# Kernel optimization log

Hardware: AMD Instinct MI355X
Metric: run time of the kernel (lower is better)

## Reference

```python
import jax, jax.numpy as jnp
import numpy as np

B, S, H, A = 64, 200, 256, 16
CAPS_LAYERS = 3
NEG = -1e9
LN_EPS = 1e-12


def _layernorm(x, g, b):
    mu = jnp.mean(x, axis=-1, keepdims=True)
    var = jnp.mean(jnp.square(x - mu), axis=-1, keepdims=True)
    return (x - mu) / jnp.sqrt(var + LN_EPS) * g + b


def setup_inputs() -> dict:
    key = jax.random.key(0)
    ks = jax.random.split(key, 10)
    s = 0.02  # initializer_range
    return {
        "item_emb": jax.random.normal(ks[0], (B, S, H), jnp.float32),
        "item_seq": jax.random.randint(ks[1], (B, S), 0, 50000),
        "time_seq": jax.random.randint(ks[2], (B, S, 2), 0, 14),
        "W_lin": s * jax.random.normal(ks[3], (H, H), jnp.float32),
        "b_lin": jnp.zeros((H,), jnp.float32),
        "aspect_embs": s * jax.random.normal(ks[4], (A, H), jnp.float32),
        "pos_emb": s * jax.random.normal(ks[5], (S, H), jnp.float32),
        "tdt_emb": s * jax.random.normal(ks[6], (14, H), jnp.float32),
        "tdn_emb": s * jax.random.normal(ks[7], (14, H), jnp.float32),
        "Wa1": s * jax.random.normal(ks[8], (H, H), jnp.float32),
        "ba1": jnp.zeros((H,), jnp.float32),
        "Wa2": s * jax.random.normal(ks[9], (H,), jnp.float32),
        "ba2": jnp.zeros((1,), jnp.float32),
        "ln_g": jnp.ones((H,), jnp.float32),
        "ln_b": jnp.zeros((H,), jnp.float32),
    }


def reference(item_emb, item_seq, time_seq, W_lin, b_lin, aspect_embs,
              pos_emb, tdt_emb, tdn_emb, Wa1, ba1, Wa2, ba2, ln_g, ln_b):
    b, s = item_emb.shape[0], item_emb.shape[1]
    pad = item_seq == 0  # [B,S]

    # ---- TimeAwareAttention (seq_output has a singleton neighbor dim in torch) ----
    td = tdt_emb[time_seq[:, :, 0]] + tdn_emb[time_seq[:, :, 1]]       # [B,S,H]
    tma_in = pos_emb[None, :s] + item_emb + td                          # [B,S,H]
    h = tma_in @ Wa1 + ba1
    h = jnp.where(h >= 0, h, 0.01 * h)                                  # LeakyReLU
    w = h @ Wa2 + ba2[0]                                                # [B,S]
    w = jnp.where(pad, NEG, w)
    tma = jax.nn.softmax(w, axis=-1)                                    # [B,S]

    # ---- gating (eval: clean gates) ----
    gates = jnp.einsum('bsh,ah->bsa', item_emb, aspect_embs)            # [B,S,A]
    idx = jnp.argmax(gates, axis=-1)                                    # topk k=1, [B,S]

    src = jnp.where(pad, 0.0, 1.0)
    counts = jnp.zeros((b, A), jnp.float32).at[jnp.arange(b)[:, None], idx].add(src)
    aspect_mask = counts == 0                                           # [B,A]

    # ---- item transform (dropout = identity in eval) ----
    moe = _layernorm(jnp.tanh(item_emb @ W_lin + b_lin) + item_emb, ln_g, ln_b)  # [B,S,H]

    # ---- capsule routing ----
    bij = gates
    cap = jnp.broadcast_to(aspect_embs[None], (b, A, H))
    for _ in range(CAPS_LAYERS):
        cij = jnp.where(aspect_mask[:, None, :], NEG, bij)
        cij = jax.nn.softmax(cij, axis=-1)
        cij = jnp.where(pad[:, :, None], 0.0, cij)                      # [B,S,A]
        cap = jnp.einsum('bsa,bsh,bs->bah', cij, moe, tma)              # [B,A,H]
        n2 = jnp.sum(jnp.square(cap), axis=-1, keepdims=True)
        cap = n2 / (1.0 + n2) / jnp.sqrt(n2 + 1e-9) * cap               # squash
        bij = bij + jnp.einsum('bsh,bah->bsa', moe, cap)

    # ---- gather activated interests / activation positions ----
    activated = cap[jnp.arange(b)[:, None], idx]                        # [B,S,H]
    seq_pos = jnp.where(pad, 0, jnp.arange(1, s + 1)[None, :]).astype(jnp.float32)
    act_mat = jnp.full((b, s, A), -1.0, jnp.float32)
    act_mat = act_mat.at[jnp.arange(b)[:, None], jnp.arange(s)[None, :], idx].set(seq_pos)
    act_mat = jnp.where(pad[:, :, None], -1.0, act_mat)
    max_pos = jnp.max(act_mat, axis=1)                                  # [B,A]
    aspects_item_idx = jnp.where(max_pos > -1.0, max_pos - 1.0, max_pos)

    gates_sm = jax.nn.softmax(gates, axis=-1)
    return (cap, gates_sm, aspect_mask, activated, aspects_item_idx, idx[:, :, None])
```

## Files before the change

### kernel.cpp

```cpp
#include <hip/hip_runtime.h>

#define B_ 64
#define S_ 200
#define H_ 256
#define A_ 16
#define M_ (B_*S_)
#define NEGV (-1000000000.0f)

typedef unsigned short ushortT;
typedef __attribute__((ext_vector_type(8))) short short8;
typedef __attribute__((ext_vector_type(4))) float f32x4;

__device__ __forceinline__ ushortT bf16u(float f) {
  unsigned int u = __builtin_bit_cast(unsigned int, f);
  unsigned int r = (u + 0x7fffu + ((u >> 16) & 1u)) >> 16;
  return (ushortT)r;
}
__device__ __forceinline__ float bf2f(ushortT u) {
  unsigned int v = ((unsigned int)u) << 16;
  return __builtin_bit_cast(float, v);
}

__global__ __launch_bounds__(256) void prep_kernel(
    const float* __restrict__ item, const float* __restrict__ Wa1,
    const float* __restrict__ W_lin, const float* __restrict__ asp,
    ushortT* __restrict__ Wa1T, ushortT* __restrict__ WlinT,
    float* __restrict__ graw, float* __restrict__ gates_sm,
    float* __restrict__ idxf)
{
  const int blk = blockIdx.x;
  const int t = threadIdx.x;

  if (blk >= 800) {
    __shared__ float T[64*65];
    int wsel = (blk - 800) >> 4;
    int tile = (blk - 800) & 15;
    const float* W = wsel ? W_lin : Wa1;
    ushortT* WT = wsel ? WlinT : Wa1T;
    int tr = (tile >> 2) * 64, tc = (tile & 3) * 64;
    #pragma unroll
    for (int p = 0; p < 16; ++p) {
      int r = p*4 + (t >> 6);
      int c = t & 63;
      T[c*65 + r] = W[(tr + r)*H_ + tc + c];
    }
    __syncthreads();
    #pragma unroll
    for (int p = 0; p < 16; ++p) {
      int n = p*4 + (t >> 6);
      int k = t & 63;
      WT[(tc + n)*H_ + tr + k] = bf16u(T[n*65 + k]);
    }
    return;
  }

  __shared__ float aspl[16*260];
  __shared__ float gL[16*20];

  const int m0 = blk * 16;
  #pragma unroll
  for (int i = 0; i < 4; ++i) {
    int e = t + 256*i;
    int r = e >> 6, c = e & 63;
    *(float4*)&aspl[r*260 + 4*c] = *(const float4*)&asp[r*H_ + 4*c];
  }
  __syncthreads();

  {
    int r = t >> 4, a = t & 15;
    int m = m0 + r;
    float g = 0.f;
    #pragma unroll 4
    for (int k4 = 0; k4 < 64; ++k4) {
      float4 xv = *(const float4*)&item[(size_t)m*H_ + 4*k4];
      float4 av = *(const float4*)&aspl[a*260 + 4*k4];
      g += xv.x*av.x + xv.y*av.y + xv.z*av.z + xv.w*av.w;
    }
    gL[r*20 + a] = g;
  }
  __syncthreads();
  if (t < 64) {
    int r = t >> 2, q = t & 3;
    float4 gv;
    gv.x = gL[r*20 + 4*q + 0]; gv.y = gL[r*20 + 4*q + 1];
    gv.z = gL[r*20 + 4*q + 2]; gv.w = gL[r*20 + 4*q + 3];
    *(float4*)&graw[(m0+r)*A_ + 4*q] = gv;
  }
  if (t < 16) {
    int r = t;
    float best = gL[r*20]; int bi = 0;
    float mx = gL[r*20];
    #pragma unroll
    for (int a = 1; a < 16; ++a) {
      float v = gL[r*20 + a];
      if (v > best) { best = v; bi = a; }
      mx = fmaxf(mx, v);
    }
    idxf[m0 + r] = (float)bi;
    float ex[16]; float sm = 0.f;
    #pragma unroll
    for (int a = 0; a < 16; ++a) { ex[a] = expf(gL[r*20 + a] - mx); sm += ex[a]; }
    float inv = 1.f / sm;
    #pragma unroll
    for (int a = 0; a < 16; ++a) gates_sm[(m0+r)*A_ + a] = ex[a]*inv;
  }
}

#define ASTR 280
#define BSTR 40
__global__ __launch_bounds__(512) void gemm_kernel(
    const float* __restrict__ item, const int* __restrict__ iseq,
    const int* __restrict__ tseq, const float* __restrict__ pos,
    const float* __restrict__ tdt, const float* __restrict__ tdn,
    const ushortT* __restrict__ Wa1T, const ushortT* __restrict__ WlinT,
    const float* __restrict__ ba1, const float* __restrict__ Wa2,
    const float* __restrict__ ba2, const float* __restrict__ b_lin,
    const float* __restrict__ g_ln, const float* __restrict__ b_ln,
    float* __restrict__ w_out, ushortT* __restrict__ moe_outB)
{
  __shared__ ushortT Atma[64*ASTR];
  __shared__ ushortT Aitm[64*ASTR];
  __shared__ ushortT B0l[256*BSTR];
  __shared__ ushortT B1l[256*BSTR];
  __shared__ int sL[64], ttL[64], tnL[64];
  __shared__ float wp[2][64];
  __shared__ float ln1[2][64], ln2[2][64];
  __shared__ float mus[64], rss[64];

  const int t = threadIdx.x;
  const int m0 = blockIdx.x * 64;
  const int lane = t & 63, w = t >> 6;
  const int g = w >> 2, wl = w & 3;
  const int wm = wl >> 1, wn = wl & 1;
  const int col = lane & 15;
  const int rg  = lane >> 4;

  if (t < 64) {
    int m = m0 + t;
    sL[t]  = m % S_;
    ttL[t] = tseq[2*m];
    tnL[t] = tseq[2*m+1];
  }
  __syncthreads();

  const int arow = t >> 3;
  const int ac4  = (t & 7) * 4;
  const int nr   = t >> 1;
  const int kh   = (t & 1) * 16;
  const int srow = sL[arow], trow = ttL[arow], nrow = tnL[arow];

  float4 pi = *(const float4*)&item[(size_t)(m0+arow)*H_ + ac4];
  float4 pp = *(const float4*)&pos[srow*H_ + ac4];
  float4 pt = *(const float4*)&tdt[trow*H_ + ac4];
  float4 pn = *(const float4*)&tdn[nrow*H_ + ac4];
  uint4 b0a = *(const uint4*)&Wa1T[(size_t)nr*H_ + kh];
  uint4 b0b = *(const uint4*)&Wa1T[(size_t)nr*H_ + kh + 8];
  uint4 b1a = *(const uint4*)&WlinT[(size_t)nr*H_ + kh];
  uint4 b1b = *(const uint4*)&WlinT[(size_t)nr*H_ + kh + 8];

  f32x4 acc[2][8];
  #pragma unroll
  for (int r = 0; r < 2; ++r)
    #pragma unroll
    for (int q = 0; q < 8; ++q) acc[r][q] = (f32x4){0.f,0.f,0.f,0.f};

  #pragma unroll
  for (int ks = 0; ks < 8; ++ks) {
    const int k0 = ks*32;
    union { ushortT u[4]; uint2 v; } ci, ct;
    ci.u[0] = bf16u(pi.x); ci.u[1] = bf16u(pi.y);
    ci.u[2] = bf16u(pi.z); ci.u[3] = bf16u(pi.w);
    ct.u[0] = bf16u(pi.x + pp.x + pt.x + pn.x);
    ct.u[1] = bf16u(pi.y + pp.y + pt.y + pn.y);
    ct.u[2] = bf16u(pi.z + pp.z + pt.z + pn.z);
    ct.u[3] = bf16u(pi.w + pp.w + pt.w + pn.w);
    *(uint2*)&Aitm[arow*ASTR + k0 + ac4] = ci.v;
    *(uint2*)&Atma[arow*ASTR + k0 + ac4] = ct.v;
    *(uint4*)&B0l[nr*BSTR + kh]     = b0a;
    *(uint4*)&B0l[nr*BSTR + kh + 8] = b0b;
    *(uint4*)&B1l[nr*BSTR + kh]     = b1a;
    *(uint4*)&B1l[nr*BSTR + kh + 8] = b1b;
    if (ks < 7) {
      const int k1 = k0 + 32;
      pi = *(const float4*)&item[(size_t)(m0+arow)*H_ + k1 + ac4];
      pp = *(const float4*)&pos[srow*H_ + k1 + ac4];
      pt = *(const float4*)&tdt[trow*H_ + k1 + ac4];
      pn = *(const float4*)&tdn[nrow*H_ + k1 + ac4];
      b0a = *(const uint4*)&Wa1T[(size_t)nr*H_ + k1 + kh];
      b0b = *(const uint4*)&Wa1T[(size_t)nr*H_ + k1 + kh + 8];
      b1a = *(const uint4*)&WlinT[(size_t)nr*H_ + k1 + kh];
      b1b = *(const uint4*)&WlinT[(size_t)nr*H_ + k1 + kh + 8];
    }
    __syncthreads();
    const ushortT* Ab = g ? Aitm : Atma;
    const ushortT* Bb = g ? B1l : B0l;
    short8 af0 = *(const short8*)&Ab[(wm*32 + col)*ASTR + k0 + rg*8];
    short8 af1 = *(const short8*)&Ab[(wm*32 + 16 + col)*ASTR + k0 + rg*8];
    #pragma unroll
    for (int q = 0; q < 8; ++q) {
      short8 bf = *(const short8*)&Bb[(wn*128 + q*16 + col)*BSTR + rg*8];
      acc[0][q] = __builtin_amdgcn_mfma_f32_16x16x32_bf16(af0, bf, acc[0][q], 0, 0, 0);
      acc[1][q] = __builtin_amdgcn_mfma_f32_16x16x32_bf16(af1, bf, acc[1][q], 0, 0, 0);
    }
    if (ks < 7) __syncthreads();
  }

  float glv[8], bbv[8];
  if (g == 0) {
    float bav[8], wav[8];
    #pragma unroll
    for (int q = 0; q < 8; ++q) {
      int n = wn*128 + q*16 + col;
      bav[q] = ba1[n]; wav[q] = Wa2[n];
    }
    #pragma unroll
    for (int r = 0; r < 2; ++r)
      #pragma unroll
      for (int j = 0; j < 4; ++j) {
        float p = 0.f;
        #pragma unroll
        for (int q = 0; q < 8; ++q) {
          float h = acc[r][q][j] + bav[q];
          h = (h >= 0.f) ? h : 0.01f*h;
          p += h * wav[q];
        }
        #pragma unroll
        for (int mk = 1; mk < 16; mk <<= 1) p += __shfl_xor(p, mk);
        if (col == 0) wp[wn][wm*32 + r*16 + rg*4 + j] = p;
      }
  } else {
    float blv[8];
    #pragma unroll
    for (int q = 0; q < 8; ++q) {
      int n = wn*128 + q*16 + col;
      blv[q] = b_lin[n]; glv[q] = g_ln[n]; bbv[q] = b_ln[n];
    }
    #pragma unroll
    for (int r = 0; r < 2; ++r)
      #pragma unroll
      for (int j = 0; j < 4; ++j) {
        int row = wm*32 + r*16 + rg*4 + j;
        float s1 = 0.f, s2 = 0.f;
        #pragma unroll
        for (int q = 0; q < 8; ++q) {
          int n = wn*128 + q*16 + col;
          float vv = tanhf(acc[r][q][j] + blv[q]) + bf2f(Aitm[row*ASTR + n]);
          acc[r][q][j] = vv; s1 += vv; s2 += vv*vv;
        }
        #pragma unroll
        for (int mk = 1; mk < 16; mk <<= 1) {
          s1 += __shfl_xor(s1, mk);
          s2 += __shfl_xor(s2, mk);
        }
        if (col == 0) { ln1[wn][row] = s1; ln2[wn][row] = s2; }
      }
  }
  __syncthreads();
  if (t < 64) {
    int row = t, m = m0 + row;
    w_out[m] = (iseq[m] == 0) ? NEGV : (wp[0][row] + wp[1][row] + ba2[0]);
  } else if (t < 128) {
    int row = t - 64;
    float s1 = ln1[0][row] + ln1[1][row];
    float s2 = ln2[0][row] + ln2[1][row];
    float mu  = s1 * (1.0f/H_);
    float var = s2 * (1.0f/H_) - mu*mu;
    mus[row] = mu;
    rss[row] = 1.0f / sqrtf(fmaxf(var, 0.f) + 1e-12f);
  }
  __syncthreads();
  if (g == 1) {
    #pragma unroll
    for (int r = 0; r < 2; ++r)
      #pragma unroll
      for (int j = 0; j < 4; ++j) {
        int row = wm*32 + r*16 + rg*4 + j;
        int m = m0 + row;
        float mu = mus[row], rs = rss[row];
        #pragma unroll
        for (int q = 0; q < 8; ++q) {
          int n = wn*128 + q*16 + col;
          moe_outB[(size_t)m*H_ + n] = bf16u((acc[r][q][j] - mu)*rs*glv[q] + bbv[q]);
        }
      }
  }
}

__device__ __forceinline__ float blk_max(float v, float* red) {
  #pragma unroll
  for (int mk = 32; mk; mk >>= 1) v = fmaxf(v, __shfl_xor(v, mk));
  int t = threadIdx.x;
  if ((t & 63) == 0) red[t >> 6] = v;
  __syncthreads();
  if (t < 64) {
    float x = (t < 16) ? red[t] : -3.0e38f;
    #pragma unroll
    for (int mk = 8; mk; mk >>= 1) x = fmaxf(x, __shfl_xor(x, mk));
    if (t == 0) red[0] = x;
  }
  __syncthreads();
  float r = red[0];
  __syncthreads();
  return r;
}

__device__ __forceinline__ float blk_sum(float v, float* red) {
  #pragma unroll
  for (int mk = 32; mk; mk >>= 1) v += __shfl_xor(v, mk);
  int t = threadIdx.x;
  if ((t & 63) == 0) red[t >> 6] = v;
  __syncthreads();
  if (t < 64) {
    float x = (t < 16) ? red[t] : 0.f;
    #pragma unroll
    for (int mk = 8; mk; mk >>= 1) x += __shfl_xor(x, mk);
    if (t == 0) red[0] = x;
  }
  __syncthreads();
  float r = red[0];
  __syncthreads();
  return r;
}

#define WGSTR 232
#define CBSTR 260
#define CLSTR 252

__global__ __launch_bounds__(1024) void phaseC_kernel(
    const int* __restrict__ iseq, const float* __restrict__ w_in,
    const ushortT* __restrict__ moeB, const float* __restrict__ idxf,
    const float* __restrict__ graw,
    float* __restrict__ cap_out,
    float* __restrict__ mask_out,
    float* __restrict__ aidx_out)
{
  __shared__ ushortT moeTr[57344];
  __shared__ ushortT wgtT[16*WGSTR];
  __shared__ ushortT capB[16*CBSTR];
  __shared__ float bij[4032];
  __shared__ float n2p[16*17];
  __shared__ float n2s[16];
  __shared__ float tmaL[S_];
  __shared__ float red[16];
  __shared__ float maskf[A_];
  __shared__ int counts[A_], maxpos[A_];
  __shared__ int idxl[S_];
  __shared__ int padl[S_];

  const int t = threadIdx.x;
  const int b = blockIdx.x;
  const int base = b * S_;
  const int lane = t & 63, w = t >> 6;
  const int la = lane & 15, lg = lane >> 4;

  #pragma unroll
  for (int u = 0; u < 4; ++u) {
    int e = t + 1024*u;
    if (e < 3584) {
      int ht = e & 15, s = e >> 4;
      int ks = s >> 5, s4l = (s >> 2) & 7, sr = s & 3;
      int bp = (s4l & 1) ? 4 + (s4l >> 1) : (s4l >> 1);
      int li = ((ht*7 + ks)*8 + bp)*64 + sr*16;
      if (s < S_) {
        const ushortT* gp = &moeB[((size_t)(base + s))*H_ + ht*16];
        *(uint4*)&moeTr[li]     = *(const uint4*)gp;
        *(uint4*)&moeTr[li + 8] = *(const uint4*)(gp + 8);
      } else {
        uint4 z = {0,0,0,0};
        *(uint4*)&moeTr[li] = z; *(uint4*)&moeTr[li + 8] = z;
      }
    }
  }
  if (t < 512) {
    int a = t >> 5, s = 200 + (t & 31);
    wgtT[a*WGSTR + s] = 0;
  }

  if (t < A_) { counts[t] = 0; maxpos[t] = -1; }
  float wv = -3.0e38f;
  if (t < S_) {
    int s = t;
    padl[s] = (iseq[base+s] == 0) ? 1 : 0;
    idxl[s] = (int)idxf[base+s];
    wv = w_in[base+s];
    #pragma unroll
    for (int q = 0; q < 4; ++q)
      *(float4*)&bij[s*20 + 4*q] = *(const float4*)&graw[(base+s)*A_ + 4*q];
  }
  __syncthreads();

  if (t < S_ && !padl[t]) {
    atomicAdd(&counts[idxl[t]], 1);
    atomicMax(&maxpos[idxl[t]], t + 1);
  }
  float mxw = blk_max(wv, red);
  float ev = (t < S_) ? expf(wv - mxw) : 0.f;
  float sw = blk_sum(ev, red);
  if (t < S_) tmaL[t] = ev / sw;
  __syncthreads();
  if (t < A_) {
    int c = counts[t];
    float mkv = (c == 0) ? 1.f : 0.f;
    maskf[t] = mkv;
    mask_out[b*A_ + t] = mkv;
    int mp = maxpos[t];
    aidx_out[b*A_ + t] = (mp > 0) ? (float)(mp - 1) : -1.f;
  }
  __syncthreads();

  for (int iter = 0; iter < 3; ++iter) {
    if (t < S_) {
      int s = t;
      float row[16]; float mx = -3.0e38f;
      #pragma unroll
      for (int a = 0; a < 16; ++a) {
        float v = bij[s*20+a];
        v = (maskf[a] > 0.5f) ? NEGV : v;
        row[a] = v; mx = fmaxf(mx, v);
      }
      float sm = 0.f;
      #pragma unroll
      for (int a = 0; a < 16; ++a) { row[a] = expf(row[a] - mx); sm += row[a]; }
      float sc = (padl[s] ? 0.f : tmaL[s]) / sm;
      #pragma unroll
      for (int a = 0; a < 16; ++a) wgtT[a*WGSTR + s] = bf16u(row[a]*sc);
    }
    __syncthreads();

    f32x4 acc = (f32x4){0.f,0.f,0.f,0.f};
    {
      unsigned vA = (unsigned)(w*7168 + lane*8);
      #pragma unroll
      for (int ks = 0; ks < 7; ++ks) {
        unsigned vAk = vA + (unsigned)(ks*1024);
        long long r0, r1;
        asm volatile(
          "ds_read_b64_tr_b16 %0, %2\n\t"
          "ds_read_b64_tr_b16 %1, %2 offset:512\n\t"
          "s_waitcnt lgkmcnt(0)"
          : "=&v"(r0), "=&v"(r1) : "v"(vAk) : "memory");
        __builtin_amdgcn_sched_barrier(0);
        union { short8 v; long long q[2]; } uu;
        uu.q[0] = r0; uu.q[1] = r1;
        short8 bf = *(const short8*)&wgtT[la*WGSTR + ks*32 + lg*8];
        acc = __builtin_amdgcn_mfma_f32_16x16x32_bf16(uu.v, bf, acc, 0, 0, 0);
      }
    }
    {
      float n2 = acc[0]*acc[0] + acc[1]*acc[1] + acc[2]*acc[2] + acc[3]*acc[3];
      n2 += __shfl_xor(n2, 16);
      n2 += __shfl_xor(n2, 32);
      if (lane < 16) n2p[w*17 + lane] = n2;
    }
    __syncthreads();
    if (t < 16) {
      float sv = 0.f;
      #pragma unroll
      for (int w2 = 0; w2 < 16; ++w2) sv += n2p[w2*17 + t];
      n2s[t] = sv / (1.f + sv) / sqrtf(sv + 1e-9f);
    }
    __syncthreads();
    {
      float sc = n2s[la];
      if (iter < 2) {
        #pragma unroll
        for (int r = 0; r < 4; ++r)
          capB[la*CBSTR + w*16 + lg*4 + r] = bf16u(acc[r]*sc);
      } else {
        float* capl = bij;
        #pragma unroll
        for (int r = 0; r < 4; ++r)
          capl[la*CLSTR + w*16 + lg*4 + r] = acc[r]*sc;
      }
    }
    __syncthreads();

    if (iter < 2) {
      if (w < 13) {
        int sR = w*16 + la;
        int ksS = sR >> 5, s4l = (sR >> 2) & 7, sr = sR & 3;
        int bp = (s4l & 1) ? 4 + (s4l >> 1) : (s4l >> 1);
        int laneA = ksS*512 + bp*64 + sr*16 + (lg & 1)*8 + (lg >> 1)*3584;
        f32x4 accS = (f32x4){0.f,0.f,0.f,0.f};
        #pragma unroll
        for (int k4 = 0; k4 < 8; ++k4) {
          short8 am = *(const short8*)&moeTr[laneA + k4*7168];
          short8 bc = *(const short8*)&capB[la*CBSTR + k4*32 + lg*8];
          accS = __builtin_amdgcn_mfma_f32_16x16x32_bf16(am, bc, accS, 0, 0, 0);
        }
        int sW = w*16 + lg*4;
        #pragma unroll
        for (int r = 0; r < 4; ++r)
          if (sW + r < S_) bij[(sW + r)*20 + la] += accS[r];
      }
      __syncthreads();
    }
  }

  {
    const float* capl = bij;
    int a = t >> 6, h4 = t & 63;
    float4 v = *(const float4*)&capl[a*CLSTR + 4*h4];
    *(float4*)&cap_out[((size_t)b*A_ + a)*H_ + 4*h4] = v;
  }
}

__global__ __launch_bounds__(256) void gather_kernel(
    const float* __restrict__ capv, const float* __restrict__ idxf,
    float* __restrict__ act)
{
  int e4 = blockIdx.x * 256 + threadIdx.x;
  int m = e4 >> 6, h4 = e4 & 63;
  int b = m / S_;
  int id = (int)idxf[m];
  float4 v = *(const float4*)&capv[((b*A_) + id)*H_ + 4*h4];
  *(float4*)&act[(size_t)4*e4] = v;
}

extern "C" void kernel_launch(void* const* d_in, const int* in_sizes, int n_in,
                              void* d_out, int out_size, void* d_ws, size_t ws_size,
                              hipStream_t stream) {
  (void)in_sizes; (void)n_in; (void)out_size; (void)ws_size;
  const float* item  = (const float*)d_in[0];
  const int*   iseq  = (const int*)d_in[1];
  const int*   tseq  = (const int*)d_in[2];
  const float* W_lin = (const float*)d_in[3];
  const float* b_lin = (const float*)d_in[4];
  const float* asp   = (const float*)d_in[5];
  const float* pos   = (const float*)d_in[6];
  const float* tdt   = (const float*)d_in[7];
  const float* tdn   = (const float*)d_in[8];
  const float* Wa1   = (const float*)d_in[9];
  const float* ba1   = (const float*)d_in[10];
  const float* Wa2   = (const float*)d_in[11];
  const float* ba2   = (const float*)d_in[12];
  const float* g_ln  = (const float*)d_in[13];
  const float* b_ln  = (const float*)d_in[14];

  float* out    = (float*)d_out;
  float* cap_o  = out;
  float* gate_o = out + 262144;
  float* mask_o = out + 466944;
  float* act_o  = out + 467968;
  float* aidx_o = out + 3744768;
  float* idx_o  = out + 3745792;

  ushortT* moeB  = (ushortT*)d_ws;
  ushortT* Wa1T  = (ushortT*)((char*)d_ws + 6553600);
  ushortT* WlinT = (ushortT*)((char*)d_ws + 6553600 + 131072);
  float*   w_ws  = (float*)((char*)d_ws + 6553600 + 262144);
  float*   graw  = (float*)((char*)d_ws + 6553600 + 262144 + 51200);

  prep_kernel<<<832, 256, 0, stream>>>(item, Wa1, W_lin, asp,
      Wa1T, WlinT, graw, gate_o, idx_o);
  gemm_kernel<<<200, 512, 0, stream>>>(item, iseq, tseq, pos, tdt, tdn,
      Wa1T, WlinT, ba1, Wa2, ba2, b_lin, g_ln, b_ln, w_ws, moeB);
  phaseC_kernel<<<B_, 1024, 0, stream>>>(iseq, w_ws, moeB, idx_o, graw,
      cap_o, mask_o, aidx_o);
  gather_kernel<<<(M_*H_/4)/256, 256, 0, stream>>>(cap_o, idx_o, act_o);
}
```

Measured before the change: 58.80 us.

## Merge gating into GEMM launch, double-buffer B tiles, hoist capsule A-fragments

Splits the weight transpose into a small kernel and folds the gating/argmax/softmax work into the GEMM launch as extra blocks, so gating runs concurrently with the GEMM instead of in a separate pre-pass. The GEMM main loop double-buffers the B tiles, needing one barrier per k-step instead of two. The routing kernel loads its transposed moe fragments once before the three iterations rather than every iteration, and computes the per-row softmax with 16-lane shuffles instead of one thread per row. This costs more LDS per block and more registers in phaseC.

After: 60.33 us. 2.6% more time.

```diff
diff --git a/kernel.cpp b/kernel.cpp
--- a/kernel.cpp
+++ b/kernel.cpp
@@ -21,113 +21,108 @@
   return __builtin_bit_cast(float, v);
 }
 
-__global__ __launch_bounds__(256) void prep_kernel(
-    const float* __restrict__ item, const float* __restrict__ Wa1,
-    const float* __restrict__ W_lin, const float* __restrict__ asp,
-    ushortT* __restrict__ Wa1T, ushortT* __restrict__ WlinT,
+__global__ __launch_bounds__(256) void prepT_kernel(
+    const float* __restrict__ Wa1, const float* __restrict__ W_lin,
+    ushortT* __restrict__ Wa1T, ushortT* __restrict__ WlinT)
+{
+  __shared__ float T[64*65];
+  const int blk = blockIdx.x, t = threadIdx.x;
+  int wsel = blk >> 4;
+  int tile = blk & 15;
+  const float* W = wsel ? W_lin : Wa1;
+  ushortT* WT = wsel ? WlinT : Wa1T;
+  int tr = (tile >> 2) * 64, tc = (tile & 3) * 64;
+  #pragma unroll
+  for (int p = 0; p < 16; ++p) {
+    int r = p*4 + (t >> 6);
+    int c = t & 63;
+    T[c*65 + r] = W[(tr + r)*H_ + tc + c];
+  }
+  __syncthreads();
+  #pragma unroll
+  for (int p = 0; p < 16; ++p) {
+    int n = p*4 + (t >> 6);
+    int k = t & 63;
+    WT[(tc + n)*H_ + tr + k] = bf16u(T[n*65 + k]);
+  }
+}
+
+#define ASTR 264
+__global__ __launch_bounds__(512) void gemmx_kernel(
+    const float* __restrict__ item, const int* __restrict__ iseq,
+    const int* __restrict__ tseq, const float* __restrict__ pos,
+    const float* __restrict__ tdt, const float* __restrict__ tdn,
+    const float* __restrict__ asp,
+    const ushortT* __restrict__ Wa1T, const ushortT* __restrict__ WlinT,
+    const float* __restrict__ ba1, const float* __restrict__ Wa2,
+    const float* __restrict__ ba2, const float* __restrict__ b_lin,
+    const float* __restrict__ g_ln, const float* __restrict__ b_ln,
+    float* __restrict__ w_out, ushortT* __restrict__ moe_outB,
     float* __restrict__ graw, float* __restrict__ gates_sm,
     float* __restrict__ idxf)
 {
-  const int blk = blockIdx.x;
+  __shared__ __align__(16) ushortT smem[74752];
+  __shared__ int sL[64], ttL[64], tnL[64];
+  __shared__ float wp[2][64], ln1[2][64], ln2[2][64], mus[64], rss[64];
+
   const int t = threadIdx.x;
 
-  if (blk >= 800) {
-    __shared__ float T[64*65];
-    int wsel = (blk - 800) >> 4;
-    int tile = (blk - 800) & 15;
-    const float* W = wsel ? W_lin : Wa1;
-    ushortT* WT = wsel ? WlinT : Wa1T;
-    int tr = (tile >> 2) * 64, tc = (tile & 3) * 64;
-    #pragma unroll
-    for (int p = 0; p < 16; ++p) {
-      int r = p*4 + (t >> 6);
-      int c = t & 63;
-      T[c*65 + r] = W[(tr + r)*H_ + tc + c];
-    }
-    __syncthreads();
-    #pragma unroll
-    for (int p = 0; p < 16; ++p) {
-      int n = p*4 + (t >> 6);
-      int k = t & 63;
-      WT[(tc + n)*H_ + tr + k] = bf16u(T[n*65 + k]);
-    }
-    return;
-  }
-
-  __shared__ float aspl[16*260];
-  __shared__ float gL[16*20];
-
-  const int m0 = blk * 16;
-  #pragma unroll
-  for (int i = 0; i < 4; ++i) {
-    int e = t + 256*i;
-    int r = e >> 6, c = e & 63;
-    *(float4*)&aspl[r*260 + 4*c] = *(const float4*)&asp[r*H_ + 4*c];
-  }
-  __syncthreads();
-
-  {
-    int r = t >> 4, a = t & 15;
-    int m = m0 + r;
+  if (blockIdx.x >= 200) {
+    float* aspl = (float*)smem;
+    float* gLs  = aspl + 16*260;
+    const int m0 = (blockIdx.x - 200) * 32;
+    #pragma unroll
+    for (int i = 0; i < 2; ++i) {
+      int e = t + 512*i;
+      int r = e >> 6, c = e & 63;
+      *(float4*)&aspl[r*260 + 4*c] = *(const float4*)&asp[r*H_ + 4*c];
+    }
+    __syncthreads();
+    const int r = t >> 4, a = t & 15;
+    const int m = m0 + r;
     float g = 0.f;
-    #pragma unroll 4
+    #pragma unroll 8
     for (int k4 = 0; k4 < 64; ++k4) {
       float4 xv = *(const float4*)&item[(size_t)m*H_ + 4*k4];
       float4 av = *(const float4*)&aspl[a*260 + 4*k4];
       g += xv.x*av.x + xv.y*av.y + xv.z*av.z + xv.w*av.w;
     }
-    gL[r*20 + a] = g;
-  }
-  __syncthreads();
-  if (t < 64) {
-    int r = t >> 2, q = t & 3;
-    float4 gv;
-    gv.x = gL[r*20 + 4*q + 0]; gv.y = gL[r*20 + 4*q + 1];
-    gv.z = gL[r*20 + 4*q + 2]; gv.w = gL[r*20 + 4*q + 3];
-    *(float4*)&graw[(m0+r)*A_ + 4*q] = gv;
-  }
-  if (t < 16) {
-    int r = t;
-    float best = gL[r*20]; int bi = 0;
-    float mx = gL[r*20];
-    #pragma unroll
-    for (int a = 1; a < 16; ++a) {
-      float v = gL[r*20 + a];
-      if (v > best) { best = v; bi = a; }
-      mx = fmaxf(mx, v);
-    }
-    idxf[m0 + r] = (float)bi;
-    float ex[16]; float sm = 0.f;
-    #pragma unroll
-    for (int a = 0; a < 16; ++a) { ex[a] = expf(gL[r*20 + a] - mx); sm += ex[a]; }
-    float inv = 1.f / sm;
-    #pragma unroll
-    for (int a = 0; a < 16; ++a) gates_sm[(m0+r)*A_ + a] = ex[a]*inv;
-  }
-}
-
-#define ASTR 280
-#define BSTR 40
-__global__ __launch_bounds__(512) void gemm_kernel(
-    const float* __restrict__ item, const int* __restrict__ iseq,
-    const int* __restrict__ tseq, const float* __restrict__ pos,
-    const float* __restrict__ tdt, const float* __restrict__ tdn,
-    const ushortT* __restrict__ Wa1T, const ushortT* __restrict__ WlinT,
-    const float* __restrict__ ba1, const float* __restrict__ Wa2,
-    const float* __restrict__ ba2, const float* __restrict__ b_lin,
-    const float* __restrict__ g_ln, const float* __restrict__ b_ln,
-    float* __restrict__ w_out, ushortT* __restrict__ moe_outB)
-{
-  __shared__ ushortT Atma[64*ASTR];
-  __shared__ ushortT Aitm[64*ASTR];
-  __shared__ ushortT B0l[256*BSTR];
-  __shared__ ushortT B1l[256*BSTR];
-  __shared__ int sL[64], ttL[64], tnL[64];
-  __shared__ float wp[2][64];
-  __shared__ float ln1[2][64], ln2[2][64];
-  __shared__ float mus[64], rss[64];
-
-  const int t = threadIdx.x;
+    gLs[r*20 + a] = g;
+    __syncthreads();
+    if (t < 128) {
+      int rr = t >> 2, q = t & 3;
+      float4 gv;
+      gv.x = gLs[rr*20 + 4*q + 0]; gv.y = gLs[rr*20 + 4*q + 1];
+      gv.z = gLs[rr*20 + 4*q + 2]; gv.w = gLs[rr*20 + 4*q + 3];
+      *(float4*)&graw[(m0+rr)*A_ + 4*q] = gv;
+    }
+    {
+      float v = g;
+      float mx = v;
+      #pragma unroll
+      for (int mk = 1; mk < 16; mk <<= 1) mx = fmaxf(mx, __shfl_xor(mx, mk));
+      float e = expf(v - mx);
+      float sm = e;
+      #pragma unroll
+      for (int mk = 1; mk < 16; mk <<= 1) sm += __shfl_xor(sm, mk);
+      gates_sm[(size_t)m*A_ + a] = e / sm;
+    }
+    if (t < 32) {
+      float best = gLs[t*20]; int bi = 0;
+      #pragma unroll
+      for (int aa = 1; aa < 16; ++aa) {
+        float v = gLs[t*20 + aa];
+        if (v > best) { best = v; bi = aa; }
+      }
+      idxf[m0 + t] = (float)bi;
+    }
+    return;
+  }
+
+  ushortT* Atma = smem;
+  ushortT* Aitm = smem + 16896;
+  ushortT* Bbuf = smem + 33792;
+
   const int m0 = blockIdx.x * 64;
   const int lane = t & 63, w = t >> 6;
   const int g = w >> 2, wl = w & 3;
@@ -164,9 +159,7 @@
     #pragma unroll
     for (int q = 0; q < 8; ++q) acc[r][q] = (f32x4){0.f,0.f,0.f,0.f};
 
-  #pragma unroll
-  for (int ks = 0; ks < 8; ++ks) {
-    const int k0 = ks*32;
+  {
     union { ushortT u[4]; uint2 v; } ci, ct;
     ci.u[0] = bf16u(pi.x); ci.u[1] = bf16u(pi.y);
     ci.u[2] = bf16u(pi.z); ci.u[3] = bf16u(pi.w);
@@ -174,12 +167,18 @@
     ct.u[1] = bf16u(pi.y + pp.y + pt.y + pn.y);
     ct.u[2] = bf16u(pi.z + pp.z + pt.z + pn.z);
     ct.u[3] = bf16u(pi.w + pp.w + pt.w + pn.w);
-    *(uint2*)&Aitm[arow*ASTR + k0 + ac4] = ci.v;
-    *(uint2*)&Atma[arow*ASTR + k0 + ac4] = ct.v;
-    *(uint4*)&B0l[nr*BSTR + kh]     = b0a;
-    *(uint4*)&B0l[nr*BSTR + kh + 8] = b0b;
-    *(uint4*)&B1l[nr*BSTR + kh]     = b1a;
-    *(uint4*)&B1l[nr*BSTR + kh + 8] = b1b;
+    *(uint2*)&Aitm[arow*ASTR + ac4] = ci.v;
+    *(uint2*)&Atma[arow*ASTR + ac4] = ct.v;
+    *(uint4*)&Bbuf[0*10240 + nr*40 + kh]     = b0a;
+    *(uint4*)&Bbuf[0*10240 + nr*40 + kh + 8] = b0b;
+    *(uint4*)&Bbuf[2*10240 + nr*40 + kh]     = b1a;
+    *(uint4*)&Bbuf[2*10240 + nr*40 + kh + 8] = b1b;
+  }
+  __syncthreads();
+
+  #pragma unroll
+  for (int ks = 0; ks < 8; ++ks) {
+    const int k0 = ks*32;
     if (ks < 7) {
       const int k1 = k0 + 32;
       pi = *(const float4*)&item[(size_t)(m0+arow)*H_ + k1 + ac4];
@@ -191,18 +190,36 @@
       b1a = *(const uint4*)&WlinT[(size_t)nr*H_ + k1 + kh];
       b1b = *(const uint4*)&WlinT[(size_t)nr*H_ + k1 + kh + 8];
     }
-    __syncthreads();
-    const ushortT* Ab = g ? Aitm : Atma;
-    const ushortT* Bb = g ? B1l : B0l;
-    short8 af0 = *(const short8*)&Ab[(wm*32 + col)*ASTR + k0 + rg*8];
-    short8 af1 = *(const short8*)&Ab[(wm*32 + 16 + col)*ASTR + k0 + rg*8];
-    #pragma unroll
-    for (int q = 0; q < 8; ++q) {
-      short8 bf = *(const short8*)&Bb[(wn*128 + q*16 + col)*BSTR + rg*8];
-      acc[0][q] = __builtin_amdgcn_mfma_f32_16x16x32_bf16(af0, bf, acc[0][q], 0, 0, 0);
-      acc[1][q] = __builtin_amdgcn_mfma_f32_16x16x32_bf16(af1, bf, acc[1][q], 0, 0, 0);
-    }
-    if (ks < 7) __syncthreads();
+    {
+      const ushortT* Ab = g ? Aitm : Atma;
+      const ushortT* Bb = Bbuf + (g*2 + (ks & 1))*10240;
+      short8 af0 = *(const short8*)&Ab[(wm*32 + col)*ASTR + k0 + rg*8];
+      short8 af1 = *(const short8*)&Ab[(wm*32 + 16 + col)*ASTR + k0 + rg*8];
+      #pragma unroll
+      for (int q = 0; q < 8; ++q) {
+        short8 bf = *(const short8*)&Bb[(wn*128 + q*16 + col)*40 + rg*8];
+        acc[0][q] = __builtin_amdgcn_mfma_f32_16x16x32_bf16(af0, bf, acc[0][q], 0, 0, 0);
+        acc[1][q] = __builtin_amdgcn_mfma_f32_16x16x32_bf16(af1, bf, acc[1][q], 0, 0, 0);
+      }
+    }
+    if (ks < 7) {
+      const int k1 = k0 + 32;
+      const int p = (ks + 1) & 1;
+      union { ushortT u[4]; uint2 v; } ci, ct;
+      ci.u[0] = bf16u(pi.x); ci.u[1] = bf16u(pi.y);
+      ci.u[2] = bf16u(pi.z); ci.u[3] = bf16u(pi.w);
+      ct.u[0] = bf16u(pi.x + pp.x + pt.x + pn.x);
+      ct.u[1] = bf16u(pi.y + pp.y + pt.y + pn.y);
+      ct.u[2] = bf16u(pi.z + pp.z + pt.z + pn.z);
+      ct.u[3] = bf16u(pi.w + pp.w + pt.w + pn.w);
+      *(uint2*)&Aitm[arow*ASTR + k1 + ac4] = ci.v;
+      *(uint2*)&Atma[arow*ASTR + k1 + ac4] = ct.v;
+      *(uint4*)&Bbuf[(0*2+p)*10240 + nr*40 + kh]     = b0a;
+      *(uint4*)&Bbuf[(0*2+p)*10240 + nr*40 + kh + 8] = b0b;
+      *(uint4*)&Bbuf[(1*2+p)*10240 + nr*40 + kh]     = b1a;
+      *(uint4*)&Bbuf[(1*2+p)*10240 + nr*40 + kh + 8] = b1b;
+    }
+    __syncthreads();
   }
 
   float glv[8], bbv[8];
@@ -389,6 +406,24 @@
   }
   __syncthreads();
 
+  short8 a2[7];
+  {
+    unsigned vA = (unsigned)(w*7168 + lane*8);
+    #pragma unroll
+    for (int ks = 0; ks < 7; ++ks) {
+      long long r0, r1;
+      asm volatile(
+        "ds_read_b64_tr_b16 %0, %2\n\t"
+        "ds_read_b64_tr_b16 %1, %2 offset:512\n\t"
+        "s_waitcnt lgkmcnt(0)"
+        : "=&v"(r0), "=&v"(r1) : "v"(vA + (unsigned)(ks*1024)) : "memory");
+      __builtin_amdgcn_sched_barrier(0);
+      union { short8 v; long long q[2]; } uu;
+      uu.q[0] = r0; uu.q[1] = r1;
+      a2[ks] = uu.v;
+    }
+  }
+
   if (t < S_ && !padl[t]) {
     atomicAdd(&counts[idxl[t]], 1);
     atomicMax(&maxpos[idxl[t]], t + 1);
@@ -409,42 +444,31 @@
   __syncthreads();
 
   for (int iter = 0; iter < 3; ++iter) {
-    if (t < S_) {
-      int s = t;
-      float row[16]; float mx = -3.0e38f;
-      #pragma unroll
-      for (int a = 0; a < 16; ++a) {
-        float v = bij[s*20+a];
+    #pragma unroll
+    for (int pass = 0; pass < 4; ++pass) {
+      int s = pass*64 + (t >> 4);
+      int a = t & 15;
+      if (s < S_) {
+        float v = bij[s*20 + a];
         v = (maskf[a] > 0.5f) ? NEGV : v;
-        row[a] = v; mx = fmaxf(mx, v);
-      }
-      float sm = 0.f;
-      #pragma unroll
-      for (int a = 0; a < 16; ++a) { row[a] = expf(row[a] - mx); sm += row[a]; }
-      float sc = (padl[s] ? 0.f : tmaL[s]) / sm;
-      #pragma unroll
-      for (int a = 0; a < 16; ++a) wgtT[a*WGSTR + s] = bf16u(row[a]*sc);
+        float mx = v;
+        #pragma unroll
+        for (int mk = 1; mk < 16; mk <<= 1) mx = fmaxf(mx, __shfl_xor(mx, mk));
+        float e = expf(v - mx);
+        float sm = e;
+        #pragma unroll
+        for (int mk = 1; mk < 16; mk <<= 1) sm += __shfl_xor(sm, mk);
+        float sc = (padl[s] ? 0.f : tmaL[s]) / sm;
+        wgtT[a*WGSTR + s] = bf16u(e*sc);
+      }
     }
     __syncthreads();
 
     f32x4 acc = (f32x4){0.f,0.f,0.f,0.f};
-    {
-      unsigned vA = (unsigned)(w*7168 + lane*8);
-      #pragma unroll
-      for (int ks = 0; ks < 7; ++ks) {
-        unsigned vAk = vA + (unsigned)(ks*1024);
-        long long r0, r1;
-        asm volatile(
-          "ds_read_b64_tr_b16 %0, %2\n\t"
-          "ds_read_b64_tr_b16 %1, %2 offset:512\n\t"
-          "s_waitcnt lgkmcnt(0)"
-          : "=&v"(r0), "=&v"(r1) : "v"(vAk) : "memory");
-        __builtin_amdgcn_sched_barrier(0);
-        union { short8 v; long long q[2]; } uu;
-        uu.q[0] = r0; uu.q[1] = r1;
-        short8 bf = *(const short8*)&wgtT[la*WGSTR + ks*32 + lg*8];
-        acc = __builtin_amdgcn_mfma_f32_16x16x32_bf16(uu.v, bf, acc, 0, 0, 0);
-      }
+    #pragma unroll
+    for (int ks = 0; ks < 7; ++ks) {
+      short8 bf = *(const short8*)&wgtT[la*WGSTR + ks*32 + lg*8];
+      acc = __builtin_amdgcn_mfma_f32_16x16x32_bf16(a2[ks], bf, acc, 0, 0, 0);
     }
     {
       float n2 = acc[0]*acc[0] + acc[1]*acc[1] + acc[2]*acc[2] + acc[3]*acc[3];
@@ -551,10 +575,10 @@
   float*   w_ws  = (float*)((char*)d_ws + 6553600 + 262144);
   float*   graw  = (float*)((char*)d_ws + 6553600 + 262144 + 51200);
 
-  prep_kernel<<<832, 256, 0, stream>>>(item, Wa1, W_lin, asp,
-      Wa1T, WlinT, graw, gate_o, idx_o);
-  gemm_kernel<<<200, 512, 0, stream>>>(item, iseq, tseq, pos, tdt, tdn,
-      Wa1T, WlinT, ba1, Wa2, ba2, b_lin, g_ln, b_ln, w_ws, moeB);
+  prepT_kernel<<<32, 256, 0, stream>>>(Wa1, W_lin, Wa1T, WlinT);
+  gemmx_kernel<<<600, 512, 0, stream>>>(item, iseq, tseq, pos, tdt, tdn, asp,
+      Wa1T, WlinT, ba1, Wa2, ba2, b_lin, g_ln, b_ln, w_ws, moeB,
+      graw, gate_o, idx_o);
   phaseC_kernel<<<B_, 1024, 0, stream>>>(iseq, w_ws, moeB, idx_o, graw,
       cap_o, mask_o, aidx_o);
   gather_kernel<<<(M_*H_/4)/256, 256, 0, stream>>>(cap_o, idx_o, act_o);
```
